# Kernel optimization log

Hardware: AMD Instinct MI355X
Metric: run time of the kernel (lower is better)

The kernel has to match this reference:

```python
import math
import jax, jax.numpy as jnp
import numpy as np

BATCH, SEQ, EMBED, HEADS = 2, 2048, 1024, 16
HEAD_DIM = EMBED // HEADS


def setup_inputs() -> dict:
    key = jax.random.key(0)
    k1, k2, k3 = jax.random.split(key, 3)
    scale = 1.0 / math.sqrt(EMBED)  # keep pre-softmax logits in a sane range
    x = jax.random.normal(k1, (BATCH, SEQ, EMBED), dtype=jnp.float32)
    mask = jnp.ones((BATCH, SEQ), dtype=jnp.int32)
    qkv_w = jax.random.normal(k2, (3 * EMBED, EMBED), dtype=jnp.float32) * scale
    out_w = jax.random.normal(k3, (EMBED, EMBED), dtype=jnp.float32) * scale
    out_b = jnp.zeros((EMBED,), dtype=jnp.float32)
    return {"x": x, "mask": mask, "qkv_w": qkv_w, "out_w": out_w, "out_b": out_b}


def reference(x, mask, qkv_w, out_w, out_b):
    b, s, e = x.shape
    # qkv projection (torch Linear: x @ W.T), then split heads
    qkv = (x @ qkv_w.T).reshape(b, s, 3, HEADS, HEAD_DIM)
    q, k, v = qkv[:, :, 0], qkv[:, :, 1], qkv[:, :, 2]  # each [b,s,h,d]
    # full score matrix [b,h,s,s]
    scores = jnp.einsum('bshd,bthd->bhst', q, k) / math.sqrt(HEAD_DIM)
    # mask broadcast over query dim and heads: [b,1,1,s_keys]
    scores = jnp.where(mask[:, None, None, :] == 0, -jnp.inf, scores)
    attn = jax.nn.softmax(scores, axis=-1)
    # dropout is identity in eval mode
    out = jnp.einsum('bhst,bthd->bshd', attn, v).reshape(b, s, e)
    return out @ out_w.T + out_b
```

## Files before the change

kernel.cpp:

```cpp
#include <hip/hip_runtime.h>
#include <hip/hip_bf16.h>

#define BATCH 2
#define SEQ   2048
#define EMBED 1024
#define HEADS 16
#define HDIM  64
#define NBH   (BATCH*HEADS)

typedef __attribute__((ext_vector_type(8))) short short8;
typedef __attribute__((ext_vector_type(4))) float floatx4;
typedef unsigned short u16;
typedef unsigned int   u32;

__device__ __forceinline__ void async_cp16(const void* g, void* l) {
  __builtin_amdgcn_global_load_lds((const __attribute__((address_space(1))) void*)g,
                                   (__attribute__((address_space(3))) void*)l,
                                   16, 0, 0);
}

__device__ __forceinline__ u16 f2b(float f) {
  union { float f; u32 u; } x; x.f = f;
  return (u16)((x.u + 0x7fffu + ((x.u >> 16) & 1u)) >> 16);
}
__device__ __forceinline__ u32 pk2(float a, float b) {
  __hip_bfloat162 t = __float22bfloat162_rn(make_float2(a, b));
  return *reinterpret_cast<u32*>(&t);
}

__global__ __launch_bounds__(256)
void cvt_all(const float* __restrict__ x, const float* __restrict__ wqkv,
             const float* __restrict__ wo,
             u16* __restrict__ xb, u16* __restrict__ wqkvb, u16* __restrict__ wob) {
  const size_t t = (size_t)blockIdx.x * 256 + threadIdx.x;
  const float* src; u16* dst; size_t off;
  if (t < 1048576) { src = x; dst = xb; off = t; }
  else if (t < 1048576 + 786432) { src = wqkv; dst = wqkvb; off = t - 1048576; }
  else { src = wo; dst = wob; off = t - (1048576 + 786432); }
  float4 v = *(const float4*)(src + off * 4);
  ushort4 o;
  o.x = f2b(v.x); o.y = f2b(v.y); o.z = f2b(v.z); o.w = f2b(v.w);
  *(ushort4*)(dst + off * 4) = o;
}

__global__ __launch_bounds__(256, 3)
void qkv_gemm(const u16* __restrict__ X, const u16* __restrict__ W,
              u16* __restrict__ q_ws, u16* __restrict__ k_ws,
              u16* __restrict__ vT_ws) {
  __shared__ u16 As[4][128][8];
  __shared__ u16 Bs[4][128][8];
  const int tid  = threadIdx.x;
  const int lane = tid & 63, wv = tid >> 6;
  const int l15  = lane & 15, quad = lane >> 4;
  const int wm = (wv >> 1) << 6, wn = (wv & 1) << 6;
  const int m0 = blockIdx.y << 7, n0 = blockIdx.x << 7;
  const bool vpath = (n0 >= 2048);

  floatx4 acc[4][4];
#pragma unroll
  for (int i = 0; i < 4; ++i)
#pragma unroll
    for (int j = 0; j < 4; ++j) acc[i][j] = {0.f, 0.f, 0.f, 0.f};

  if (!vpath) {
    for (int k0 = 0; k0 < EMBED; k0 += 32) {
      __syncthreads();
#pragma unroll
      for (int i = 0; i < 2; ++i) {
        int c = tid + (i << 8);
        int kb = c >> 7, row = c & 127;
        async_cp16(X + (size_t)(m0 + row) * EMBED + k0 + kb * 8, &As[kb][row][0]);
        async_cp16(W + (size_t)(n0 + row) * EMBED + k0 + kb * 8, &Bs[kb][row][0]);
      }
      __syncthreads();

      short8 af[4], bf[4];
#pragma unroll
      for (int t = 0; t < 4; ++t) {
        af[t] = *(const short8*)&As[quad][wm + t * 16 + l15][0];
        bf[t] = *(const short8*)&Bs[quad][wn + t * 16 + l15][0];
      }
#pragma unroll
      for (int i = 0; i < 4; ++i)
#pragma unroll
        for (int j = 0; j < 4; ++j)
          acc[i][j] = __builtin_amdgcn_mfma_f32_16x16x32_bf16(bf[j], af[i], acc[i][j], 0, 0, 0);
    }

#pragma unroll
    for (int i = 0; i < 4; ++i) {
      int mg = m0 + wm + i * 16 + l15;
      int b = mg >> 11, s = mg & 2047;
#pragma unroll
      for (int j = 0; j < 4; ++j) {
        int col0 = n0 + wn + j * 16 + (quad << 2);
        int c = col0 >> 10, hd = col0 & 1023;
        int h = hd >> 6, d0 = hd & 63;
        u16* dst = c ? k_ws : q_ws;
        uint2 w;
        w.x = pk2(acc[i][j][0], acc[i][j][1]);
        w.y = pk2(acc[i][j][2], acc[i][j][3]);
        *(uint2*)(dst + (((size_t)(b * HEADS + h)) * SEQ + s) * HDIM + d0) = w;
      }
    }
  } else {
    for (int k0 = 0; k0 < EMBED; k0 += 32) {
      __syncthreads();
#pragma unroll
      for (int i = 0; i < 2; ++i) {
        int c = tid + (i << 8);
        int kb = c >> 7, row = c & 127;
        async_cp16(X + (size_t)(m0 + row) * EMBED + k0 + kb * 8, &As[kb][row][0]);
        async_cp16(W + (size_t)(n0 + row) * EMBED + k0 + kb * 8, &Bs[kb][row][0]);
      }
      __syncthreads();

      short8 af[4], bf[4];
#pragma unroll
      for (int t = 0; t < 4; ++t) {
        af[t] = *(const short8*)&As[quad][wm + t * 16 + l15][0];
        bf[t] = *(const short8*)&Bs[quad][wn + t * 16 + l15][0];
      }
#pragma unroll
      for (int i = 0; i < 4; ++i)
#pragma unroll
        for (int j = 0; j < 4; ++j)
          acc[i][j] = __builtin_amdgcn_mfma_f32_16x16x32_bf16(af[i], bf[j], acc[i][j], 0, 0, 0);
    }

#pragma unroll
    for (int i = 0; i < 4; ++i) {
      int mg0 = m0 + wm + i * 16 + (quad << 2);
      int b = mg0 >> 11, s0 = mg0 & 2047;
#pragma unroll
      for (int j = 0; j < 4; ++j) {
        int col = n0 + wn + j * 16 + l15;
        int hd = col & 1023;
        int h = hd >> 6, d = hd & 63;
        uint2 w;
        w.x = pk2(acc[i][j][0], acc[i][j][1]);
        w.y = pk2(acc[i][j][2], acc[i][j][3]);
        *(uint2*)(vT_ws + (((size_t)(b * HEADS + h)) * HDIM + d) * SEQ + s0) = w;
      }
    }
  }
}

__global__ __launch_bounds__(256, 4)
void attn_kernel(const u16* __restrict__ q_ws, const u16* __restrict__ k_ws,
                 const u16* __restrict__ vT_ws, const int* __restrict__ mask,
                 u16* __restrict__ ao) {
  __shared__ u16 Ks[8][64][8];
  __shared__ u16 Vt[8][64][8];
  __shared__ u16 Ps[4][16][68];
  __shared__ float msk[64];

  const int tid  = threadIdx.x;
  const int lane = tid & 63, wv = tid >> 6;
  const int l15  = lane & 15, quad = lane >> 4;
  const int bh = blockIdx.y;
  const int b  = bh >> 4, h = bh & 15;
  const int qrw = (blockIdx.x << 6) + (wv << 4);

  const u16* Qb  = q_ws  + (size_t)bh * SEQ * HDIM;
  const u16* Kb  = k_ws  + (size_t)bh * SEQ * HDIM;
  const u16* VbT = vT_ws + (size_t)bh * HDIM * SEQ;

  short8 qf[2];
#pragma unroll
  for (int s = 0; s < 2; ++s) {
    short8 v = *(const short8*)(Qb + (size_t)(qrw + l15) * HDIM + s * 32 + quad * 8);
#pragma unroll
    for (int e = 0; e < 8; ++e) {
      union { float f; u32 u; } x;
      x.u = ((u32)(u16)v[e]) << 16;
      x.f *= 0.125f;
      v[e] = (short)(x.u >> 16);
    }
    qf[s] = v;
  }

  float m_run = -1e30f, l_run = 0.f;
  floatx4 O[4];
#pragma unroll
  for (int dt = 0; dt < 4; ++dt) O[dt] = {0.f, 0.f, 0.f, 0.f};

  for (int t0 = 0; t0 < SEQ; t0 += 64) {
    __syncthreads();
#pragma unroll
    for (int i = 0; i < 2; ++i) {
      int c = tid + (i << 8);
      int kb = c >> 6, r = c & 63;
      async_cp16(Kb + (size_t)(t0 + r) * HDIM + kb * 8, &Ks[kb][r][0]);
      async_cp16(VbT + (size_t)r * SEQ + t0 + kb * 8, &Vt[kb][r][0]);
    }
    if (tid < 64) msk[tid] = mask[b * SEQ + t0 + tid] ? 0.f : -1e30f;
    __syncthreads();

    floatx4 sc[4];
#pragma unroll
    for (int nt = 0; nt < 4; ++nt) {
      sc[nt] = {0.f, 0.f, 0.f, 0.f};
#pragma unroll
      for (int s = 0; s < 2; ++s) {
        short8 kf = *(const short8*)&Ks[s * 4 + quad][nt * 16 + l15][0];
        sc[nt] = __builtin_amdgcn_mfma_f32_16x16x32_bf16(kf, qf[s], sc[nt], 0, 0, 0);
      }
    }

    float mt = -1e30f;
#pragma unroll
    for (int nt = 0; nt < 4; ++nt) {
      const float4 m4 = *(const float4*)&msk[nt * 16 + quad * 4];
#pragma unroll
      for (int r = 0; r < 4; ++r) {
        sc[nt][r] += (&m4.x)[r];
        mt = fmaxf(mt, sc[nt][r]);
      }
    }
    mt = fmaxf(mt, __shfl_xor(mt, 16));
    mt = fmaxf(mt, __shfl_xor(mt, 32));

    const float mn = fmaxf(m_run, mt);
    const float al = __expf(m_run - mn);
    m_run = mn;

    float rs = 0.f;
#pragma unroll
    for (int nt = 0; nt < 4; ++nt) {
      float pv[4];
#pragma unroll
      for (int r = 0; r < 4; ++r) { pv[r] = __expf(sc[nt][r] - mn); rs += pv[r]; }
      uint2 w;
      w.x = pk2(pv[0], pv[1]); w.y = pk2(pv[2], pv[3]);
      *(uint2*)&Ps[wv][l15][nt * 16 + (quad << 2)] = w;
    }
    rs += __shfl_xor(rs, 16);
    rs += __shfl_xor(rs, 32);
    l_run = l_run * al + rs;

#pragma unroll
    for (int dt = 0; dt < 4; ++dt)
#pragma unroll
      for (int r = 0; r < 4; ++r) O[dt][r] *= al;

#pragma unroll
    for (int tch = 0; tch < 2; ++tch) {
      short8 pf = *(const short8*)&Ps[wv][l15][tch * 32 + quad * 8];
#pragma unroll
      for (int dt = 0; dt < 4; ++dt) {
        short8 vf = *(const short8*)&Vt[tch * 4 + quad][dt * 16 + l15][0];
        O[dt] = __builtin_amdgcn_mfma_f32_16x16x32_bf16(vf, pf, O[dt], 0, 0, 0);
      }
    }
  }

  const float inv = 1.f / l_run;
  const size_t rowbase = ((size_t)(b * SEQ + qrw + l15)) * EMBED + h * 64;
#pragma unroll
  for (int dt = 0; dt < 4; ++dt) {
    uint2 w;
    w.x = pk2(O[dt][0] * inv, O[dt][1] * inv);
    w.y = pk2(O[dt][2] * inv, O[dt][3] * inv);
    *(uint2*)(ao + rowbase + dt * 16 + (quad << 2)) = w;
  }
}

__global__ __launch_bounds__(256, 2)
void proj_gemm(const u16* __restrict__ A, const u16* __restrict__ W,
               const float* __restrict__ bias, float* __restrict__ out) {
  __shared__ u16 As[4][128][8];
  __shared__ u16 Bs[4][64][8];
  const int tid  = threadIdx.x;
  const int lane = tid & 63, wv = tid >> 6;
  const int l15  = lane & 15, quad = lane >> 4;
  const int wm = (wv >> 1) << 6, wn = (wv & 1) << 5;
  const int m0 = blockIdx.y << 7, n0 = blockIdx.x << 6;

  floatx4 acc[4][2];
#pragma unroll
  for (int i = 0; i < 4; ++i)
#pragma unroll
    for (int j = 0; j < 2; ++j) acc[i][j] = {0.f, 0.f, 0.f, 0.f};

  for (int k0 = 0; k0 < EMBED; k0 += 32) {
    __syncthreads();
#pragma unroll
    for (int i = 0; i < 2; ++i) {
      int c = tid + (i << 8);
      int kb = c >> 7, row = c & 127;
      async_cp16(A + (size_t)(m0 + row) * EMBED + k0 + kb * 8, &As[kb][row][0]);
    }
    {
      int kb = tid >> 6, row = tid & 63;
      async_cp16(W + (size_t)(n0 + row) * EMBED + k0 + kb * 8, &Bs[kb][row][0]);
    }
    __syncthreads();

    short8 af[4], bf[2];
#pragma unroll
    for (int t = 0; t < 4; ++t)
      af[t] = *(const short8*)&As[quad][wm + t * 16 + l15][0];
#pragma unroll
    for (int t = 0; t < 2; ++t)
      bf[t] = *(const short8*)&Bs[quad][wn + t * 16 + l15][0];
#pragma unroll
    for (int i = 0; i < 4; ++i)
#pragma unroll
      for (int j = 0; j < 2; ++j)
        acc[i][j] = __builtin_amdgcn_mfma_f32_16x16x32_bf16(bf[j], af[i], acc[i][j], 0, 0, 0);
  }

#pragma unroll
  for (int i = 0; i < 4; ++i) {
    int m = m0 + wm + i * 16 + l15;
#pragma unroll
    for (int j = 0; j < 2; ++j) {
      int col0 = n0 + wn + j * 16 + (quad << 2);
      float4 bv = *(const float4*)(bias + col0);
      float4 o;
      o.x = acc[i][j][0] + bv.x;
      o.y = acc[i][j][1] + bv.y;
      o.z = acc[i][j][2] + bv.z;
      o.w = acc[i][j][3] + bv.w;
      *(float4*)(out + (size_t)m * EMBED + col0) = o;
    }
  }
}

extern "C" void kernel_launch(void* const* d_in, const int* in_sizes, int n_in,
                              void* d_out, int out_size, void* d_ws, size_t ws_size,
                              hipStream_t stream) {
  const float* x     = (const float*)d_in[0];
  const int*   mask  = (const int*)d_in[1];
  const float* qkv_w = (const float*)d_in[2];
  const float* out_w = (const float*)d_in[3];
  const float* out_b = (const float*)d_in[4];
  float* out = (float*)d_out;

  const size_t per = (size_t)NBH * SEQ * HDIM;
  u16* xb    = (u16*)d_ws;
  u16* wqkvb = xb + 4194304;
  u16* wob   = wqkvb + 3145728;
  u16* q_ws  = wob + 1048576;
  u16* k_ws  = q_ws + per;
  u16* vT_ws = k_ws + per;
  u16* ao    = vT_ws + per;

  cvt_all<<<8192, 256, 0, stream>>>(x, qkv_w, out_w, xb, wqkvb, wob);
  qkv_gemm<<<dim3(24, 32), 256, 0, stream>>>(xb, wqkvb, q_ws, k_ws, vT_ws);
  attn_kernel<<<dim3(SEQ / 64, NBH), 256, 0, stream>>>(q_ws, k_ws, vT_ws, mask, ao);
  proj_gemm<<<dim3(16, 32), 256, 0, stream>>>(ao, wob, out_b, out);
}
```

Before: 249.5 us.

## Use exp2 softmax, skip no-op rescale, shrink output projection tile

The attention softmax now scales scores by log2(e) and uses the hardware exp2 instruction instead of __expf. It also skips rescaling the output accumulator when no lane's running max changed. The output projection GEMM moves from 128x64 to 64x64 tiles, doubling the number of blocks and raising the occupancy hint, which trades per-block data reuse for more parallelism. The wave-wide any-check adds a branch to each iteration.

```diff
diff --git a/kernel.cpp b/kernel.cpp
--- a/kernel.cpp
+++ b/kernel.cpp
@@ -13,6 +13,8 @@
 typedef unsigned short u16;
 typedef unsigned int   u32;
 
+#define LOG2E 1.4426950408889634f
+
 __device__ __forceinline__ void async_cp16(const void* g, void* l) {
   __builtin_amdgcn_global_load_lds((const __attribute__((address_space(1))) void*)g,
                                    (__attribute__((address_space(3))) void*)l,
@@ -26,6 +28,13 @@
 __device__ __forceinline__ u32 pk2(float a, float b) {
   __hip_bfloat162 t = __float22bfloat162_rn(make_float2(a, b));
   return *reinterpret_cast<u32*>(&t);
+}
+__device__ __forceinline__ float fexp2(float x) {
+#if __has_builtin(__builtin_amdgcn_exp2f)
+  return __builtin_amdgcn_exp2f(x);
+#else
+  return __expf(x * 0.6931471805599453f);
+#endif
 }
 
 __global__ __launch_bounds__(256)
@@ -214,7 +223,7 @@
       const float4 m4 = *(const float4*)&msk[nt * 16 + quad * 4];
 #pragma unroll
       for (int r = 0; r < 4; ++r) {
-        sc[nt][r] += (&m4.x)[r];
+        sc[nt][r] = fmaf(sc[nt][r], LOG2E, (&m4.x)[r]);
         mt = fmaxf(mt, sc[nt][r]);
       }
     }
@@ -222,7 +231,7 @@
     mt = fmaxf(mt, __shfl_xor(mt, 32));
 
     const float mn = fmaxf(m_run, mt);
-    const float al = __expf(m_run - mn);
+    const float al = fexp2(m_run - mn);
     m_run = mn;
 
     float rs = 0.f;
@@ -230,7 +239,7 @@
     for (int nt = 0; nt < 4; ++nt) {
       float pv[4];
 #pragma unroll
-      for (int r = 0; r < 4; ++r) { pv[r] = __expf(sc[nt][r] - mn); rs += pv[r]; }
+      for (int r = 0; r < 4; ++r) { pv[r] = fexp2(sc[nt][r] - mn); rs += pv[r]; }
       uint2 w;
       w.x = pk2(pv[0], pv[1]); w.y = pk2(pv[2], pv[3]);
       *(uint2*)&Ps[wv][l15][nt * 16 + (quad << 2)] = w;
@@ -239,10 +248,12 @@
     rs += __shfl_xor(rs, 32);
     l_run = l_run * al + rs;
 
-#pragma unroll
-    for (int dt = 0; dt < 4; ++dt)
-#pragma unroll
-      for (int r = 0; r < 4; ++r) O[dt][r] *= al;
+    if (__any(al < 1.0f)) {
+#pragma unroll
+      for (int dt = 0; dt < 4; ++dt)
+#pragma unroll
+        for (int r = 0; r < 4; ++r) O[dt][r] *= al;
+    }
 
 #pragma unroll
     for (int tch = 0; tch < 2; ++tch) {
@@ -266,65 +277,51 @@
   }
 }
 
-__global__ __launch_bounds__(256, 2)
+__global__ __launch_bounds__(256, 4)
 void proj_gemm(const u16* __restrict__ A, const u16* __restrict__ W,
                const float* __restrict__ bias, float* __restrict__ out) {
-  __shared__ u16 As[4][128][8];
+  __shared__ u16 As[4][64][8];
   __shared__ u16 Bs[4][64][8];
   const int tid  = threadIdx.x;
   const int lane = tid & 63, wv = tid >> 6;
   const int l15  = lane & 15, quad = lane >> 4;
-  const int wm = (wv >> 1) << 6, wn = (wv & 1) << 5;
-  const int m0 = blockIdx.y << 7, n0 = blockIdx.x << 6;
-
-  floatx4 acc[4][2];
-#pragma unroll
-  for (int i = 0; i < 4; ++i)
-#pragma unroll
-    for (int j = 0; j < 2; ++j) acc[i][j] = {0.f, 0.f, 0.f, 0.f};
+  const int wm = wv << 4;
+  const int m0 = blockIdx.y << 6, n0 = blockIdx.x << 6;
+
+  floatx4 acc[4];
+#pragma unroll
+  for (int j = 0; j < 4; ++j) acc[j] = {0.f, 0.f, 0.f, 0.f};
 
   for (int k0 = 0; k0 < EMBED; k0 += 32) {
     __syncthreads();
-#pragma unroll
-    for (int i = 0; i < 2; ++i) {
-      int c = tid + (i << 8);
-      int kb = c >> 7, row = c & 127;
-      async_cp16(A + (size_t)(m0 + row) * EMBED + k0 + kb * 8, &As[kb][row][0]);
-    }
     {
       int kb = tid >> 6, row = tid & 63;
+      async_cp16(A + (size_t)(m0 + row) * EMBED + k0 + kb * 8, &As[kb][row][0]);
       async_cp16(W + (size_t)(n0 + row) * EMBED + k0 + kb * 8, &Bs[kb][row][0]);
     }
     __syncthreads();
 
-    short8 af[4], bf[2];
+    short8 af = *(const short8*)&As[quad][wm + l15][0];
+    short8 bf[4];
 #pragma unroll
     for (int t = 0; t < 4; ++t)
-      af[t] = *(const short8*)&As[quad][wm + t * 16 + l15][0];
-#pragma unroll
-    for (int t = 0; t < 2; ++t)
-      bf[t] = *(const short8*)&Bs[quad][wn + t * 16 + l15][0];
-#pragma unroll
-    for (int i = 0; i < 4; ++i)
-#pragma unroll
-      for (int j = 0; j < 2; ++j)
-        acc[i][j] = __builtin_amdgcn_mfma_f32_16x16x32_bf16(bf[j], af[i], acc[i][j], 0, 0, 0);
-  }
-
-#pragma unroll
-  for (int i = 0; i < 4; ++i) {
-    int m = m0 + wm + i * 16 + l15;
-#pragma unroll
-    for (int j = 0; j < 2; ++j) {
-      int col0 = n0 + wn + j * 16 + (quad << 2);
-      float4 bv = *(const float4*)(bias + col0);
-      float4 o;
-      o.x = acc[i][j][0] + bv.x;
-      o.y = acc[i][j][1] + bv.y;
-      o.z = acc[i][j][2] + bv.z;
-      o.w = acc[i][j][3] + bv.w;
-      *(float4*)(out + (size_t)m * EMBED + col0) = o;
-    }
+      bf[t] = *(const short8*)&Bs[quad][t * 16 + l15][0];
+#pragma unroll
+    for (int j = 0; j < 4; ++j)
+      acc[j] = __builtin_amdgcn_mfma_f32_16x16x32_bf16(bf[j], af, acc[j], 0, 0, 0);
+  }
+
+  const int m = m0 + wm + l15;
+#pragma unroll
+  for (int j = 0; j < 4; ++j) {
+    int col0 = n0 + j * 16 + (quad << 2);
+    float4 bv = *(const float4*)(bias + col0);
+    float4 o;
+    o.x = acc[j][0] + bv.x;
+    o.y = acc[j][1] + bv.y;
+    o.z = acc[j][2] + bv.z;
+    o.w = acc[j][3] + bv.w;
+    *(float4*)(out + (size_t)m * EMBED + col0) = o;
   }
 }
 
@@ -350,5 +347,5 @@
   cvt_all<<<8192, 256, 0, stream>>>(x, qkv_w, out_w, xb, wqkvb, wob);
   qkv_gemm<<<dim3(24, 32), 256, 0, stream>>>(xb, wqkvb, q_ws, k_ws, vT_ws);
   attn_kernel<<<dim3(SEQ / 64, NBH), 256, 0, stream>>>(q_ws, k_ws, vT_ws, mask, ao);
-  proj_gemm<<<dim3(16, 32), 256, 0, stream>>>(ao, wob, out_b, out);
-}
+  proj_gemm<<<dim3(16, 64), 256, 0, stream>>>(ao, wob, out_b, out);
+}
```

Result: faster. 244.6 us (-2.0%).
